# Kernel tuning notes

Measured on AMD Instinct MI355X. Metric: run time of the kernel, lower is better.

## Reference

```python
import jax, jax.numpy as jnp
import numpy as np

NUM_USERS = 100000
NUM_ITEMS = 50000
N_NODES = NUM_USERS + NUM_ITEMS
EMB_DIM = 64
TEXT_DIM = 384
N_LAYERS = 2
N_EDGES = 4800000


def setup_inputs() -> dict:
    key = jax.random.key(0)
    ks = jax.random.split(key, 12)
    text_feats = jax.random.normal(ks[0], (N_NODES, TEXT_DIM), jnp.float32)
    edge_row = jax.random.randint(ks[1], (N_EDGES,), 0, N_NODES, jnp.int32)
    edge_col = jax.random.randint(ks[2], (N_EDGES,), 0, N_NODES, jnp.int32)
    edge_val = jax.random.uniform(ks[3], (N_EDGES,), jnp.float32)
    tail_mask = jax.random.randint(ks[4], (N_NODES,), 0, 2, jnp.int32).astype(bool)
    # learned parameters (xavier-ish scaling)
    user_emb = jax.random.normal(ks[5], (NUM_USERS, EMB_DIM), jnp.float32) * 0.05
    item_emb = jax.random.normal(ks[6], (NUM_ITEMS, EMB_DIM), jnp.float32) * 0.05
    W_text = jax.random.normal(ks[7], (TEXT_DIM, EMB_DIM), jnp.float32) * (1.0 / np.sqrt(TEXT_DIM))
    b_text = jnp.zeros((EMB_DIM,), jnp.float32)
    W_fuse = jax.random.normal(ks[8], (2 * EMB_DIM, EMB_DIM), jnp.float32) * (1.0 / np.sqrt(2 * EMB_DIM))
    b_fuse = jnp.zeros((EMB_DIM,), jnp.float32)
    tail_amp = jnp.array(1.0, jnp.float32)
    return {
        'text_feats': text_feats, 'edge_row': edge_row, 'edge_col': edge_col,
        'edge_val': edge_val, 'tail_mask': tail_mask, 'user_emb': user_emb,
        'item_emb': item_emb, 'W_text': W_text, 'b_text': b_text,
        'W_fuse': W_fuse, 'b_fuse': b_fuse, 'tail_amp': tail_amp,
    }


def reference(text_feats, edge_row, edge_col, edge_val, tail_mask, user_emb,
              item_emb, W_text, b_text, W_fuse, b_fuse, tail_amp):
    # --- MDGRec.propagate ---
    emb_id = jnp.concatenate([user_emb, item_emb], axis=0)           # [N, D]
    emb_text = text_feats @ W_text + b_text                          # [N, D]

    def spmm(h):  # sparse adj_norm @ h via gather + segment scatter-add
        return jax.ops.segment_sum(edge_val[:, None] * h[edge_col], edge_row,
                                   num_segments=N_NODES)

    h_id, h_text = emb_id, emb_text
    sum_id, sum_text = emb_id, emb_text
    for _ in range(N_LAYERS):
        h_id = spmm(h_id)
        h_text = spmm(h_text)
        sum_id = sum_id + h_id
        sum_text = sum_text + h_text
    inv_layers = 1.0 / (N_LAYERS + 1)
    id_final = sum_id * inv_layers                                   # layer mean
    text_final = sum_text * inv_layers

    amp = 1.0 + jax.nn.sigmoid(tail_amp)
    text_final = jnp.where(tail_mask[:, None], text_final * amp, text_final)

    gate = jax.nn.sigmoid(jnp.concatenate([id_final, text_final], axis=1) @ W_fuse + b_fuse)
    fused = gate * id_final + (1.0 - gate) * text_final              # [N, D]
    return fused
```

## Files before the change

kernel.cpp:

```cpp
#include <hip/hip_runtime.h>
#include <hip/hip_bf16.h>

#define NUM_USERS 100000
#define NUM_ITEMS 50000
#define N_NODES   150000
#define EMB_DIM   64
#define TEXT_DIM  384
#define N_EDGES   4800000
#define SCAN_CHUNK 2048

__global__ __launch_bounds__(256) void zero_kernel(int* __restrict__ p, int n) {
    int i = blockIdx.x * 256 + threadIdx.x;
    if (i < n) p[i] = 0;
}

__global__ __launch_bounds__(256) void hist_kernel(const int* __restrict__ erow,
                                                   int* __restrict__ counts, int n) {
    int i = blockIdx.x * 256 + threadIdx.x;
    if (i < n) atomicAdd(&counts[erow[i]], 1);
}

__global__ __launch_bounds__(256) void scan_p1(const int* __restrict__ counts,
                                               int* __restrict__ bsums, int n) {
    __shared__ int s[256];
    int tid = threadIdx.x;
    int base = blockIdx.x * SCAN_CHUNK + tid * 8;
    int sum = 0;
#pragma unroll
    for (int j = 0; j < 8; ++j) { int idx = base + j; if (idx < n) sum += counts[idx]; }
    s[tid] = sum; __syncthreads();
    for (int off = 128; off > 0; off >>= 1) {
        if (tid < off) s[tid] += s[tid + off];
        __syncthreads();
    }
    if (tid == 0) bsums[blockIdx.x] = s[0];
}

__global__ void scan_p2(int* __restrict__ bsums, int nb) {
    if (threadIdx.x == 0 && blockIdx.x == 0) {
        int acc = 0;
        for (int i = 0; i < nb; ++i) { int v = bsums[i]; bsums[i] = acc; acc += v; }
    }
}

__global__ __launch_bounds__(256) void scan_p3(int* __restrict__ counts ,
                                               const int* __restrict__ bsums,
                                               int* __restrict__ cursor, int n) {
    __shared__ int s[256];
    int tid = threadIdx.x;
    int base = blockIdx.x * SCAN_CHUNK + tid * 8;
    int v[8]; int sum = 0;
#pragma unroll
    for (int j = 0; j < 8; ++j) { int idx = base + j; v[j] = (idx < n) ? counts[idx] : 0; sum += v[j]; }
    s[tid] = sum; __syncthreads();
    for (int off = 1; off < 256; off <<= 1) {
        int t = (tid >= off) ? s[tid - off] : 0;
        __syncthreads();
        s[tid] += t;
        __syncthreads();
    }
    int run = bsums[blockIdx.x] + (s[tid] - sum);
#pragma unroll
    for (int j = 0; j < 8; ++j) {
        int idx = base + j;
        if (idx < n) {
            counts[idx] = run;
            if (idx < N_NODES) cursor[idx] = run;
        }
        run += v[j];
    }
}

__global__ __launch_bounds__(256) void scatter_kernel(const int* __restrict__ erow,
                                                      const int* __restrict__ ecol,
                                                      const float* __restrict__ eval,
                                                      int* __restrict__ cursor,
                                                      int* __restrict__ scol,
                                                      float* __restrict__ sval, int n) {
    int i = blockIdx.x * 256 + threadIdx.x;
    if (i < n) {
        int r = erow[i];
        int pos = atomicAdd(&cursor[r], 1);
        scol[pos] = ecol[i];
        sval[pos] = eval[i];
    }
}

#define ROWS_A 16
__global__ __launch_bounds__(256) void init_kernel(const float* __restrict__ text,
                                                   const float* __restrict__ Wt,
                                                   const float* __restrict__ bt,
                                                   const float* __restrict__ uemb,
                                                   const float* __restrict__ iemb,
                                                   float* __restrict__ X) {
    __shared__ float ts[ROWS_A][TEXT_DIM];
    int t = threadIdx.x;
    int r0 = blockIdx.x * ROWS_A;
    const float4* src = (const float4*)(text + (size_t)r0 * TEXT_DIM);
    float4* dst = (float4*)&ts[0][0];
#pragma unroll
    for (int j = 0; j < 6; ++j) dst[t + j * 256] = src[t + j * 256];
    __syncthreads();
    int c = t & 63, w = t >> 6;
    float bias = bt[c];
    float acc[4];
#pragma unroll
    for (int r = 0; r < 4; ++r) acc[r] = bias;
#pragma unroll 4
    for (int k = 0; k < TEXT_DIM; ++k) {
        float wv = Wt[k * 64 + c];
#pragma unroll
        for (int r = 0; r < 4; ++r) acc[r] += wv * ts[w * 4 + r][k];
    }
#pragma unroll
    for (int r = 0; r < 4; ++r) {
        int row = r0 + w * 4 + r;
        float idv = (row < NUM_USERS) ? uemb[(size_t)row * 64 + c]
                                      : iemb[(size_t)(row - NUM_USERS) * 64 + c];
        X[(size_t)row * 128 + c] = idv;
        X[(size_t)row * 128 + 64 + c] = acc[r];
    }
}

template <int LAYER>
__global__ __launch_bounds__(256) void spmm_kernel(const float* __restrict__ src,
                                                   float* __restrict__ Y,
                                                   float* __restrict__ X,
                                                   const int* __restrict__ rstart,
                                                   const int* __restrict__ scol,
                                                   const float* __restrict__ sval) {
    int wave = threadIdx.x >> 6;
    int lane = threadIdx.x & 63;
    int row = blockIdx.x * 4 + wave;
    if (row >= N_NODES) return;
    int beg = rstart[row], end = rstart[row + 1];
    float a0 = 0.f, a1 = 0.f;
    for (int b = beg; b < end; b += 64) {
        int e = b + lane;
        int cc = 0; float vv = 0.f;
        if (e < end) { cc = scol[e]; vv = sval[e]; }
        int m = min(64, end - b);
        for (int j = 0; j < m; ++j) {
            int   cj = __shfl(cc, j);
            float vj = __shfl(vv, j);
            a0 += vj * src[(size_t)cj * 128 + lane];
            a1 += vj * src[(size_t)cj * 128 + 64 + lane];
        }
    }
    size_t o = (size_t)row * 128;
    if (LAYER == 1) {
        Y[o + lane] = a0;
        Y[o + 64 + lane] = a1;
    } else {
        X[o + lane]      += src[o + lane] + a0;
        X[o + 64 + lane] += src[o + 64 + lane] + a1;
    }
}

__global__ __launch_bounds__(256) void fuse_kernel(const float* __restrict__ X,
                                                   const float* __restrict__ Wf,
                                                   const float* __restrict__ bf,
                                                   const int* __restrict__ tmask,
                                                   const float* __restrict__ tamp,
                                                   float* __restrict__ out) {
    __shared__ float wfs[128 * 64];
    int t = threadIdx.x, c = t & 63, w = t >> 6;
    for (int j = t; j < 2048; j += 256) ((float4*)wfs)[j] = ((const float4*)Wf)[j];
    float bias = bf[c];
    float amp = 1.f + 1.f / (1.f + __expf(-tamp[0]));
    __syncthreads();
    const float inv3 = 1.f / 3.f;
    int rowbase = blockIdx.x * 256 + w * 64;
    for (int i = 0; i < 64; ++i) {
        int row = rowbase + i;
        if (row >= N_NODES) break;
        size_t o = (size_t)row * 128;
        float s1 = (tmask[row] != 0) ? inv3 * amp : inv3;
        float accA = 0.f, accB = 0.f;
#pragma unroll 8
        for (int k = 0; k < 64; ++k) accA += X[o + k] * wfs[k * 64 + c];
#pragma unroll 8
        for (int k = 0; k < 64; ++k) accB += X[o + 64 + k] * wfs[(64 + k) * 64 + c];
        float z = accA * inv3 + accB * s1 + bias;
        float g = 1.f / (1.f + __expf(-z));
        float idf = X[o + c] * inv3;
        float txf = X[o + 64 + c] * s1;
        out[(size_t)row * 64 + c] = g * idf + (1.f - g) * txf;
    }
}

extern "C" void kernel_launch(void* const* d_in, const int* in_sizes, int n_in,
                              void* d_out, int out_size, void* d_ws, size_t ws_size,
                              hipStream_t stream) {
    const float* text = (const float*)d_in[0];
    const int*   erow = (const int*)d_in[1];
    const int*   ecol = (const int*)d_in[2];
    const float* eval = (const float*)d_in[3];
    const int*   tmask= (const int*)d_in[4];
    const float* uemb = (const float*)d_in[5];
    const float* iemb = (const float*)d_in[6];
    const float* Wt   = (const float*)d_in[7];
    const float* bt   = (const float*)d_in[8];
    const float* Wf   = (const float*)d_in[9];
    const float* bf   = (const float*)d_in[10];
    const float* tamp = (const float*)d_in[11];
    float* out = (float*)d_out;

    const size_t OFF_Y      = 76800000;
    const size_t OFF_SCOL   = 153600000;
    const size_t OFF_SVAL   = 172800000;
    const size_t OFF_RSTART = 192000000;
    const size_t OFF_CURSOR = 192600064;
    const size_t OFF_BSUMS  = 193200128;
    const size_t WS_NEEDED  = OFF_BSUMS + 512;
    if (ws_size < WS_NEEDED) {
        return;
    }

    char* ws = (char*)d_ws;
    float* X      = (float*)(ws);
    float* Y      = (float*)(ws + OFF_Y);
    int*   scol   = (int*)  (ws + OFF_SCOL);
    float* sval   = (float*)(ws + OFF_SVAL);
    int*   rstart = (int*)  (ws + OFF_RSTART);
    int*   cursor = (int*)  (ws + OFF_CURSOR);
    int*   bsums  = (int*)  (ws + OFF_BSUMS);

    const int nb = (N_NODES + 1 + SCAN_CHUNK - 1) / SCAN_CHUNK;

    zero_kernel<<<(N_NODES + 1 + 255) / 256, 256, 0, stream>>>(rstart, N_NODES + 1);
    hist_kernel<<<N_EDGES / 256, 256, 0, stream>>>(erow, rstart, N_EDGES);
    scan_p1<<<nb, 256, 0, stream>>>(rstart, bsums, N_NODES + 1);
    scan_p2<<<1, 64, 0, stream>>>(bsums, nb);
    scan_p3<<<nb, 256, 0, stream>>>(rstart, bsums, cursor, N_NODES + 1);
    scatter_kernel<<<N_EDGES / 256, 256, 0, stream>>>(erow, ecol, eval, cursor, scol, sval, N_EDGES);

    init_kernel<<<N_NODES / ROWS_A, 256, 0, stream>>>(text, Wt, bt, uemb, iemb, X);

    spmm_kernel<1><<<(N_NODES + 3) / 4, 256, 0, stream>>>(X, Y, X, rstart, scol, sval);
    spmm_kernel<2><<<(N_NODES + 3) / 4, 256, 0, stream>>>(Y, Y, X, rstart, scol, sval);

    fuse_kernel<<<(N_NODES + 255) / 256, 256, 0, stream>>>(X, Wf, bf, tmask, tamp, out);
}
```

Before: 1.978 ms.

## Pack edge col/val pairs, vectorize SpMM gathers, tile fuse GEMM in shared memory

Edges are stored as interleaved (col,val) uint2 pairs, so the scatter does one 8-byte write and the SpMM does one 8-byte load per edge instead of two arrays. The SpMM gathers each neighbour row as a float2 per lane instead of two separate floats, so each lane now reads adjacent id/text columns. The fuse kernel is rewritten as a shared-memory tiled 64x128x64 GEMM with 4x4 register blocking and pre-scaled inputs, replacing per-row global reads of X. This works because X keeps id and text halves in one layout and the fuse kernel prescales each half before use.

```diff
diff --git a/kernel.cpp b/kernel.cpp
--- a/kernel.cpp
+++ b/kernel.cpp
@@ -75,14 +75,15 @@
                                                       const int* __restrict__ ecol,
                                                       const float* __restrict__ eval,
                                                       int* __restrict__ cursor,
-                                                      int* __restrict__ scol,
-                                                      float* __restrict__ sval, int n) {
+                                                      uint2* __restrict__ sedge, int n) {
     int i = blockIdx.x * 256 + threadIdx.x;
     if (i < n) {
         int r = erow[i];
         int pos = atomicAdd(&cursor[r], 1);
-        scol[pos] = ecol[i];
-        sval[pos] = eval[i];
+        uint2 e;
+        e.x = (unsigned)ecol[i];
+        e.y = __float_as_uint(eval[i]);
+        sedge[pos] = e;
     }
 }
 
@@ -127,33 +128,37 @@
                                                    float* __restrict__ Y,
                                                    float* __restrict__ X,
                                                    const int* __restrict__ rstart,
-                                                   const int* __restrict__ scol,
-                                                   const float* __restrict__ sval) {
+                                                   const uint2* __restrict__ sedge) {
     int wave = threadIdx.x >> 6;
     int lane = threadIdx.x & 63;
     int row = blockIdx.x * 4 + wave;
     if (row >= N_NODES) return;
     int beg = rstart[row], end = rstart[row + 1];
     float a0 = 0.f, a1 = 0.f;
+    const float2* s2 = (const float2*)src;
     for (int b = beg; b < end; b += 64) {
         int e = b + lane;
-        int cc = 0; float vv = 0.f;
-        if (e < end) { cc = scol[e]; vv = sval[e]; }
+        uint2 ed = make_uint2(0u, 0u);
+        if (e < end) ed = sedge[e];
         int m = min(64, end - b);
         for (int j = 0; j < m; ++j) {
-            int   cj = __shfl(cc, j);
-            float vj = __shfl(vv, j);
-            a0 += vj * src[(size_t)cj * 128 + lane];
-            a1 += vj * src[(size_t)cj * 128 + 64 + lane];
-        }
-    }
-    size_t o = (size_t)row * 128;
+            int   cj = __shfl((int)ed.x, j);
+            float vj = __shfl(__uint_as_float(ed.y), j);
+            float2 v = s2[(size_t)cj * 64 + lane];
+            a0 += vj * v.x;
+            a1 += vj * v.y;
+        }
+    }
+    size_t o2 = (size_t)row * 64 + lane;
     if (LAYER == 1) {
-        Y[o + lane] = a0;
-        Y[o + 64 + lane] = a1;
+        float2 r; r.x = a0; r.y = a1;
+        ((float2*)Y)[o2] = r;
     } else {
-        X[o + lane]      += src[o + lane] + a0;
-        X[o + 64 + lane] += src[o + 64 + lane] + a1;
+        float2 xv = ((const float2*)X)[o2];
+        float2 yv = s2[o2];
+        xv.x += yv.x + a0;
+        xv.y += yv.y + a1;
+        ((float2*)X)[o2] = xv;
     }
 }
 
@@ -163,29 +168,67 @@
                                                    const int* __restrict__ tmask,
                                                    const float* __restrict__ tamp,
                                                    float* __restrict__ out) {
-    __shared__ float wfs[128 * 64];
-    int t = threadIdx.x, c = t & 63, w = t >> 6;
-    for (int j = t; j < 2048; j += 256) ((float4*)wfs)[j] = ((const float4*)Wf)[j];
-    float bias = bf[c];
+    __shared__ float Xs[64][128];
+    __shared__ float Wfs[128][64];
+    int t = threadIdx.x;
+    int rowbase = blockIdx.x * 64;
+    const float inv3 = 1.f / 3.f;
     float amp = 1.f + 1.f / (1.f + __expf(-tamp[0]));
+
+    for (int j = t; j < 2048; j += 256) ((float4*)Wfs)[j] = ((const float4*)Wf)[j];
+#pragma unroll
+    for (int j = 0; j < 8; ++j) {
+        int f = t + j * 256;
+        int r = f >> 5;
+        int q = f & 31;
+        int row = rowbase + r;
+        float4 v = make_float4(0.f, 0.f, 0.f, 0.f);
+        if (row < N_NODES) {
+            v = ((const float4*)X)[(size_t)row * 32 + q];
+            float s = (q < 16) ? inv3 : ((tmask[row] != 0) ? inv3 * amp : inv3);
+            v.x *= s; v.y *= s; v.z *= s; v.w *= s;
+        }
+        ((float4*)Xs)[f] = v;
+    }
     __syncthreads();
-    const float inv3 = 1.f / 3.f;
-    int rowbase = blockIdx.x * 256 + w * 64;
-    for (int i = 0; i < 64; ++i) {
-        int row = rowbase + i;
+
+    int tc = t & 15, tr = t >> 4;
+    int c0 = tc * 4, r0 = tr * 4;
+    float acc[4][4];
+#pragma unroll
+    for (int i = 0; i < 4; ++i)
+#pragma unroll
+        for (int j = 0; j < 4; ++j) acc[i][j] = 0.f;
+
+    for (int k = 0; k < 128; k += 4) {
+#pragma unroll
+        for (int kk = 0; kk < 4; ++kk) {
+            float4 wv = *(const float4*)&Wfs[k + kk][c0];
+#pragma unroll
+            for (int i = 0; i < 4; ++i) {
+                float xv = Xs[r0 + i][k + kk];
+                acc[i][0] += xv * wv.x;
+                acc[i][1] += xv * wv.y;
+                acc[i][2] += xv * wv.z;
+                acc[i][3] += xv * wv.w;
+            }
+        }
+    }
+
+    float4 bq = *(const float4*)&bf[c0];
+#pragma unroll
+    for (int i = 0; i < 4; ++i) {
+        int row = rowbase + r0 + i;
         if (row >= N_NODES) break;
-        size_t o = (size_t)row * 128;
-        float s1 = (tmask[row] != 0) ? inv3 * amp : inv3;
-        float accA = 0.f, accB = 0.f;
-#pragma unroll 8
-        for (int k = 0; k < 64; ++k) accA += X[o + k] * wfs[k * 64 + c];
-#pragma unroll 8
-        for (int k = 0; k < 64; ++k) accB += X[o + 64 + k] * wfs[(64 + k) * 64 + c];
-        float z = accA * inv3 + accB * s1 + bias;
-        float g = 1.f / (1.f + __expf(-z));
-        float idf = X[o + c] * inv3;
-        float txf = X[o + 64 + c] * s1;
-        out[(size_t)row * 64 + c] = g * idf + (1.f - g) * txf;
+        float4 idf = *(const float4*)&Xs[r0 + i][c0];
+        float4 txf = *(const float4*)&Xs[r0 + i][64 + c0];
+        float4 o;
+        float g;
+        g = 1.f / (1.f + __expf(-(acc[i][0] + bq.x))); o.x = g * idf.x + (1.f - g) * txf.x;
+        g = 1.f / (1.f + __expf(-(acc[i][1] + bq.y))); o.y = g * idf.y + (1.f - g) * txf.y;
+        g = 1.f / (1.f + __expf(-(acc[i][2] + bq.z))); o.z = g * idf.z + (1.f - g) * txf.z;
+        g = 1.f / (1.f + __expf(-(acc[i][3] + bq.w))); o.w = g * idf.w + (1.f - g) * txf.w;
+        ((float4*)out)[(size_t)row * 16 + tc] = o;
     }
 }
 
@@ -207,8 +250,7 @@
     float* out = (float*)d_out;
 
     const size_t OFF_Y      = 76800000;
-    const size_t OFF_SCOL   = 153600000;
-    const size_t OFF_SVAL   = 172800000;
+    const size_t OFF_SEDGE  = 153600000;
     const size_t OFF_RSTART = 192000000;
     const size_t OFF_CURSOR = 192600064;
     const size_t OFF_BSUMS  = 193200128;
@@ -220,8 +262,7 @@
     char* ws = (char*)d_ws;
     float* X      = (float*)(ws);
     float* Y      = (float*)(ws + OFF_Y);
-    int*   scol   = (int*)  (ws + OFF_SCOL);
-    float* sval   = (float*)(ws + OFF_SVAL);
+    uint2* sedge  = (uint2*)(ws + OFF_SEDGE);
     int*   rstart = (int*)  (ws + OFF_RSTART);
     int*   cursor = (int*)  (ws + OFF_CURSOR);
     int*   bsums  = (int*)  (ws + OFF_BSUMS);
@@ -233,12 +274,12 @@
     scan_p1<<<nb, 256, 0, stream>>>(rstart, bsums, N_NODES + 1);
     scan_p2<<<1, 64, 0, stream>>>(bsums, nb);
     scan_p3<<<nb, 256, 0, stream>>>(rstart, bsums, cursor, N_NODES + 1);
-    scatter_kernel<<<N_EDGES / 256, 256, 0, stream>>>(erow, ecol, eval, cursor, scol, sval, N_EDGES);
+    scatter_kernel<<<N_EDGES / 256, 256, 0, stream>>>(erow, ecol, eval, cursor, sedge, N_EDGES);
 
     init_kernel<<<N_NODES / ROWS_A, 256, 0, stream>>>(text, Wt, bt, uemb, iemb, X);
 
-    spmm_kernel<1><<<(N_NODES + 3) / 4, 256, 0, stream>>>(X, Y, X, rstart, scol, sval);
-    spmm_kernel<2><<<(N_NODES + 3) / 4, 256, 0, stream>>>(Y, Y, X, rstart, scol, sval);
-
-    fuse_kernel<<<(N_NODES + 255) / 256, 256, 0, stream>>>(X, Wf, bf, tmask, tamp, out);
-}
+    spmm_kernel<1><<<(N_NODES + 3) / 4, 256, 0, stream>>>(X, Y, X, rstart, sedge);
+    spmm_kernel<2><<<(N_NODES + 3) / 4, 256, 0, stream>>>(Y, Y, X, rstart, sedge);
+
+    fuse_kernel<<<(N_NODES + 63) / 64, 256, 0, stream>>>(X, Wf, bf, tmask, tamp, out);
+}
```

Result: faster. 1.879 ms (-5.0%).
